# Performance work log

Measured on AMD Instinct MI355X. Metric: run time of the kernel, lower is better.

The kernel has to match this reference:

```python
import jax, jax.numpy as jnp
import numpy as np

EPS = 1e-5   # BatchNorm eps (torch default)
KNN_K = 9    # kernel_size * dilation
GROUPS = 4

def _bn(x, g, b, m, v):
    # channel-first BN in eval mode (running stats)
    shp = (1, -1) + (1,) * (x.ndim - 2)
    return (x - m.reshape(shp)) * (g.reshape(shp) * jax.lax.rsqrt(v.reshape(shp) + EPS)) + b.reshape(shp)

def setup_inputs() -> dict:
    key = jax.random.key(0)
    ks = jax.random.split(key, 16)
    B, C, H, W = 64, 192, 28, 28
    C2 = 2 * C
    d = {}
    d["x"] = jax.random.normal(ks[0], (B, C, H, W), jnp.float32)
    # fc1: Conv2d(C,C,1) + BN
    d["fc1_w"] = jax.random.normal(ks[1], (C, C), jnp.float32) * 0.05
    d["fc1_b"] = jnp.zeros((C,), jnp.float32)
    d["bn1_g"] = jnp.ones((C,), jnp.float32)
    d["bn1_b"] = jnp.zeros((C,), jnp.float32)
    d["bn1_m"] = jax.random.normal(ks[2], (C,), jnp.float32) * 0.1
    d["bn1_v"] = jax.random.uniform(ks[3], (C,), jnp.float32, 0.5, 1.5)
    # MRConv2d nn: grouped Conv2d(2C, 2C, 1, groups=4) + BN + GELU
    d["gc_w"] = jax.random.normal(ks[4], (GROUPS, C2 // GROUPS, C2 // GROUPS), jnp.float32) * 0.1  # (g, out/g, in/g)
    d["gc_b"] = jnp.zeros((C2,), jnp.float32)
    d["bn2_g"] = jnp.ones((C2,), jnp.float32)
    d["bn2_b"] = jnp.zeros((C2,), jnp.float32)
    d["bn2_m"] = jax.random.normal(ks[5], (C2,), jnp.float32) * 0.1
    d["bn2_v"] = jax.random.uniform(ks[6], (C2,), jnp.float32, 0.5, 1.5)
    # fc2: Conv2d(2C, C, 1) + BN
    d["fc2_w"] = jax.random.normal(ks[7], (C, C2), jnp.float32) * 0.05
    d["fc2_b"] = jnp.zeros((C,), jnp.float32)
    d["bn3_g"] = jnp.ones((C,), jnp.float32)
    d["bn3_b"] = jnp.zeros((C,), jnp.float32)
    d["bn3_m"] = jax.random.normal(ks[8], (C,), jnp.float32) * 0.1
    d["bn3_v"] = jax.random.uniform(ks[9], (C,), jnp.float32, 0.5, 1.5)
    return d

def reference(x, fc1_w, fc1_b, bn1_g, bn1_b, bn1_m, bn1_v,
              gc_w, gc_b, bn2_g, bn2_b, bn2_m, bn2_v,
              fc2_w, fc2_b, bn3_g, bn3_b, bn3_m, bn3_v):
    B, C, H, W = x.shape
    N = H * W
    shortcut = x
    # fc1 (1x1 conv + BN)
    h = jnp.einsum('bchw,oc->bohw', x, fc1_w) + fc1_b[None, :, None, None]
    h = _bn(h, bn1_g, bn1_b, bn1_m, bn1_v)
    xt = h.reshape(B, C, N)  # (B, C, N), r=1 so y == x.detach()
    # ---- dynamic KNN graph (no grad in original) ----
    xs = jax.lax.stop_gradient(xt)
    norm = jnp.maximum(jnp.linalg.norm(xs, axis=1, keepdims=True), 1e-12)
    xn = xs / norm                      # L2 normalize over channels
    p = jnp.swapaxes(xn, 1, 2)          # (B, N, C)
    sq = jnp.sum(p * p, axis=-1, keepdims=True)       # (B, N, 1)
    dist = sq - 2.0 * jnp.einsum('bnc,bmc->bnm', p, p) + jnp.swapaxes(sq, 1, 2)
    _, nn_idx = jax.lax.top_k(-dist, KNN_K)           # (B, N, K) smallest distances
    # ---- max-relative graph conv ----
    yd = jax.lax.stop_gradient(xt)      # neighbors come from detached y
    x_j = jax.vmap(lambda f, i: f[:, i])(yd, nn_idx)  # (B, C, N, K)
    mr = jnp.max(x_j - xt[..., None], axis=-1)        # (B, C, N)
    # interleave [x_c0, mr_c0, x_c1, mr_c1, ...] -> (B, 2C, N)
    st = jnp.stack([xt, mr], axis=2).reshape(B, 2 * C, N)
    # grouped 1x1 conv (groups=4)
    z = st.reshape(B, GROUPS, (2 * C) // GROUPS, N)
    g = jnp.einsum('bgin,goi->bgon', z, gc_w).reshape(B, 2 * C, N) + gc_b[None, :, None]
    g = _bn(g, bn2_g, bn2_b, bn2_m, bn2_v)
    g = jax.nn.gelu(g, approximate=False)
    g = g.reshape(B, 2 * C, H, W)
    # fc2 (1x1 conv + BN) + residual
    out = jnp.einsum('bchw,oc->bohw', g, fc2_w) + fc2_b[None, :, None, None]
    out = _bn(out, bn3_g, bn3_b, bn3_m, bn3_v)
    return out + shortcut
```

## Files before the change

### kernel.cpp

```cpp
#include <hip/hip_runtime.h>
#include <math.h>

static constexpr int Bn  = 64;
static constexpr int Cc  = 192;
static constexpr int Nn  = 784;
static constexpr int C2c = 384;
static constexpr int Kk  = 9;
#define GAP_DELTA 1e-4f

typedef __attribute__((ext_vector_type(8))) short bf16x8;
typedef __attribute__((ext_vector_type(4))) float f32x4;

__device__ inline unsigned short f2bf(float f) {
    unsigned int u = __float_as_uint(f);
    return (unsigned short)((u + 0x7FFFu + ((u >> 16) & 1u)) >> 16);
}


__global__ __launch_bounds__(256) void fc1_np(
    const float* __restrict__ x, const float* __restrict__ w,
    const float* __restrict__ bias,
    const float* __restrict__ gg, const float* __restrict__ bb_,
    const float* __restrict__ mm, const float* __restrict__ vv,
    float* __restrict__ xt)
{
    __shared__ float As[16][64];
    __shared__ float Bs[16][128];
    const int b   = blockIdx.z;
    const int n0  = blockIdx.x * 128;
    const int o0  = blockIdx.y * 64;
    const int tid = threadIdx.x;
    const int tx = tid & 15, ty = tid >> 4;
    const int lo = tid & 63, lk4 = tid >> 6;
    const int ln4 = tid & 15, lbk = tid >> 4;
    const float* xb = x + (size_t)b * Cc * Nn;

    float acc[4][8];
#pragma unroll
    for (int i = 0; i < 4; ++i)
#pragma unroll
        for (int j = 0; j < 8; ++j) acc[i][j] = 0.f;

    for (int kt = 0; kt < 12; ++kt) {
        const int k0 = kt * 16;
        float4 av = *reinterpret_cast<const float4*>(&w[(size_t)(o0 + lo) * 192 + k0 + lk4 * 4]);
        As[lk4*4+0][lo] = av.x;
        As[lk4*4+1][lo] = av.y;
        As[lk4*4+2][lo] = av.z;
        As[lk4*4+3][lo] = av.w;
        const int na = n0 + ln4 * 4;
        const int nb = n0 + 64 + ln4 * 4;
        float4 b0 = make_float4(0.f, 0.f, 0.f, 0.f);
        float4 b1 = make_float4(0.f, 0.f, 0.f, 0.f);
        if (na < Nn) b0 = *reinterpret_cast<const float4*>(&xb[(size_t)(k0 + lbk) * Nn + na]);
        if (nb < Nn) b1 = *reinterpret_cast<const float4*>(&xb[(size_t)(k0 + lbk) * Nn + nb]);
        *reinterpret_cast<float4*>(&Bs[lbk][ln4*4])      = b0;
        *reinterpret_cast<float4*>(&Bs[lbk][64 + ln4*4]) = b1;
        __syncthreads();
#pragma unroll
        for (int kk = 0; kk < 16; ++kk) {
            float ar[4], br[8];
#pragma unroll
            for (int i = 0; i < 4; ++i) ar[i] = As[kk][ty*4+i];
#pragma unroll
            for (int j = 0; j < 4; ++j) br[j]     = Bs[kk][tx*4+j];
#pragma unroll
            for (int j = 0; j < 4; ++j) br[4 + j] = Bs[kk][64 + tx*4+j];
#pragma unroll
            for (int i = 0; i < 4; ++i)
#pragma unroll
                for (int j = 0; j < 8; ++j)
                    acc[i][j] = __fadd_rn(acc[i][j], __fmul_rn(ar[i], br[j]));
        }
        __syncthreads();
    }
    const int na = n0 + tx * 4;
    const int nb = n0 + 64 + tx * 4;
#pragma unroll
    for (int i = 0; i < 4; ++i) {
        const int o = o0 + ty * 4 + i;
        const float e  = __fadd_rn(vv[o], 1e-5f);
        const float r1 = __fsqrt_rn(e);
        const float rr = __fdiv_rn(1.f, r1);
        const float s  = __fmul_rn(gg[o], rr);
        const size_t rowb = ((size_t)b * Cc + o) * Nn;
        if (na < Nn) {
#pragma unroll
            for (int j = 0; j < 4; ++j) {
                const float h = __fadd_rn(acc[i][j], bias[o]);
                const float t = __fsub_rn(h, mm[o]);
                const float u = __fmul_rn(t, s);
                xt[rowb + na + j] = __fadd_rn(u, bb_[o]);
            }
        }
        if (nb < Nn) {
#pragma unroll
            for (int j = 0; j < 4; ++j) {
                const float h = __fadd_rn(acc[i][4 + j], bias[o]);
                const float t = __fsub_rn(h, mm[o]);
                const float u = __fmul_rn(t, s);
                xt[rowb + nb + j] = __fadd_rn(u, bb_[o]);
            }
        }
    }
}

__global__ __launch_bounds__(256) void norm_np(
    const float* __restrict__ xt, float* __restrict__ xn, float* __restrict__ sq)
{
    const int idx = blockIdx.x * 256 + threadIdx.x;
    if (idx >= Bn * Nn) return;
    const int n = idx % Nn;
    const int b = idx / Nn;
    const float* p = xt + (size_t)b * Cc * Nn + n;

    float acc = 0.f;
    for (int c = 0; c < Cc; ++c) {
        const float v = p[(size_t)c * Nn];
        acc = __fadd_rn(acc, __fmul_rn(v, v));
    }
    float nrm = __fsqrt_rn(acc);
    nrm = fmaxf(nrm, 1e-12f);

    float* q = xn + (size_t)b * Cc * Nn + n;
    for (int c = 0; c < Cc; ++c)
        q[(size_t)c * Nn] = __fdiv_rn(p[(size_t)c * Nn], nrm);

    float sblk[2];
#pragma unroll
    for (int blk = 0; blk < 2; ++blk) {
        const int base = blk * 96;
        float r[8];
#pragma unroll
        for (int j = 0; j < 8; ++j) {
            const float xv = q[(size_t)(base + j) * Nn];
            r[j] = __fmul_rn(xv, xv);
        }
        for (int i = 8; i < 96; i += 8) {
#pragma unroll
            for (int j = 0; j < 8; ++j) {
                const float xv = q[(size_t)(base + i + j) * Nn];
                r[j] = __fadd_rn(r[j], __fmul_rn(xv, xv));
            }
        }
        sblk[blk] = __fadd_rn(__fadd_rn(__fadd_rn(r[0], r[1]), __fadd_rn(r[2], r[3])),
                              __fadd_rn(__fadd_rn(r[4], r[5]), __fadd_rn(r[6], r[7])));
    }
    sq[idx] = __fadd_rn(sblk[0], sblk[1]);
}

__global__ __launch_bounds__(256) void xpose_bf(
    const float* __restrict__ xn, unsigned short* __restrict__ xnh,
    unsigned short* __restrict__ xnl)
{
    __shared__ float T[64][65];
    const int b  = blockIdx.z;
    const int c0 = blockIdx.y * 64;
    const int n0 = blockIdx.x * 64;
    const int tid = threadIdx.x;
    const int nl = tid & 63, cq = tid >> 6;

#pragma unroll
    for (int i = 0; i < 16; ++i) {
        const int c = c0 + cq + i * 4;
        const int n = n0 + nl;
        T[cq + i*4][nl] = (n < Nn) ? xn[((size_t)b * Cc + c) * Nn + n] : 0.f;
    }
    __syncthreads();
    const int nw = tid >> 2, cpart = tid & 3;
    const int n = n0 + nw;
    if (n < Nn) {
        unsigned short hbuf[16], lbuf[16];
#pragma unroll
        for (int j = 0; j < 16; ++j) {
            const float v = T[cpart * 16 + j][nw];
            const unsigned short h = f2bf(v);
            const float hf = __uint_as_float(((unsigned int)h) << 16);
            hbuf[j] = h;
            lbuf[j] = f2bf(__fsub_rn(v, hf));
        }
        unsigned short* dh = xnh + ((size_t)b * Nn + n) * Cc + c0 + cpart * 16;
        unsigned short* dl = xnl + ((size_t)b * Nn + n) * Cc + c0 + cpart * 16;
        *reinterpret_cast<bf16x8*>(&dh[0]) = *reinterpret_cast<bf16x8*>(&hbuf[0]);
        *reinterpret_cast<bf16x8*>(&dh[8]) = *reinterpret_cast<bf16x8*>(&hbuf[8]);
        *reinterpret_cast<bf16x8*>(&dl[0]) = *reinterpret_cast<bf16x8*>(&lbuf[0]);
        *reinterpret_cast<bf16x8*>(&dl[8]) = *reinterpret_cast<bf16x8*>(&lbuf[8]);
    }
}

__global__ __launch_bounds__(256) void xpose_f32(
    const float* __restrict__ xn, float* __restrict__ xnT)
{
    __shared__ float T[64][65];
    const int b  = blockIdx.z;
    const int c0 = blockIdx.y * 64;
    const int n0 = blockIdx.x * 64;
    const int tid = threadIdx.x;
    const int nl = tid & 63, cq = tid >> 6;

#pragma unroll
    for (int i = 0; i < 16; ++i) {
        const int c = c0 + cq + i * 4;
        const int n = n0 + nl;
        T[cq + i*4][nl] = (n < Nn) ? xn[((size_t)b * Cc + c) * Nn + n] : 0.f;
    }
    __syncthreads();
    const int nw = tid >> 2, cpart = tid & 3;
    const int n = n0 + nw;
    if (n < Nn) {
        float* dst = xnT + ((size_t)b * Nn + n) * Cc + c0 + cpart * 16;
#pragma unroll
        for (int q = 0; q < 4; ++q) {
            float4 v = make_float4(T[cpart*16 + q*4 + 0][nw], T[cpart*16 + q*4 + 1][nw],
                                   T[cpart*16 + q*4 + 2][nw], T[cpart*16 + q*4 + 3][nw]);
            *reinterpret_cast<float4*>(&dst[q * 4]) = v;
        }
    }
}

__global__ __launch_bounds__(256) void dist_mfma(
    const unsigned short* __restrict__ xnh, const unsigned short* __restrict__ xnl,
    float* __restrict__ dist, int bchunk)
{
    __shared__ float Ds[64][65];
    __shared__ unsigned short Ah[64 * 40];
    __shared__ unsigned short Al[64 * 40];
    const int bt = blockIdx.x;
    int rt = 0, rem = bt;
    while (rem >= 13 - rt) { rem -= 13 - rt; ++rt; }
    const int mt = rt + rem;
    const int bc = blockIdx.y;
    const int b  = bchunk * 16 + bc;
    const int r0 = rt * 64, m0 = mt * 64;
    const int tid = threadIdx.x;
    const int wv = tid >> 6, l = tid & 63;
    const int lm = l & 15, lk = l >> 4;

    const int mcol = m0 + wv * 16 + lm;
    const int mcl  = (mcol < Nn) ? mcol : (Nn - 1);
    const unsigned short* mh = xnh + ((size_t)b * Nn + mcl) * Cc;
    const unsigned short* ml = xnl + ((size_t)b * Nn + mcl) * Cc;

    const int srow = tid >> 2, spart = tid & 3;
    const int arow = r0 + srow;
    const int arowc = (arow < Nn) ? arow : (Nn - 1);
    const unsigned short* ah_src = xnh + ((size_t)b * Nn + arowc) * Cc;
    const unsigned short* al_src = xnl + ((size_t)b * Nn + arowc) * Cc;

    f32x4 acc[4];
#pragma unroll
    for (int mf = 0; mf < 4; ++mf) acc[mf] = (f32x4){0.f, 0.f, 0.f, 0.f};

#pragma unroll
    for (int ks = 0; ks < 6; ++ks) {
        const int k0 = ks * 32;
        bf16x8 bh = *reinterpret_cast<const bf16x8*>(&mh[k0 + lk * 8]);
        bf16x8 bl = *reinterpret_cast<const bf16x8*>(&ml[k0 + lk * 8]);
        __syncthreads();
        *reinterpret_cast<bf16x8*>(&Ah[srow * 40 + spart * 8]) =
            *reinterpret_cast<const bf16x8*>(&ah_src[k0 + spart * 8]);
        *reinterpret_cast<bf16x8*>(&Al[srow * 40 + spart * 8]) =
            *reinterpret_cast<const bf16x8*>(&al_src[k0 + spart * 8]);
        __syncthreads();
#pragma unroll
        for (int mf = 0; mf < 4; ++mf) {
            bf16x8 ah = *reinterpret_cast<const bf16x8*>(&Ah[(mf * 16 + lm) * 40 + lk * 8]);
            bf16x8 al = *reinterpret_cast<const bf16x8*>(&Al[(mf * 16 + lm) * 40 + lk * 8]);
            acc[mf] = __builtin_amdgcn_mfma_f32_16x16x32_bf16(ah, bh, acc[mf], 0, 0, 0);
            acc[mf] = __builtin_amdgcn_mfma_f32_16x16x32_bf16(ah, bl, acc[mf], 0, 0, 0);
            acc[mf] = __builtin_amdgcn_mfma_f32_16x16x32_bf16(al, bh, acc[mf], 0, 0, 0);
        }
    }
    float* db = dist + (size_t)bc * Nn * Nn;
    __syncthreads();
#pragma unroll
    for (int mf = 0; mf < 4; ++mf) {
#pragma unroll
        for (int r = 0; r < 4; ++r) {
            const int rl = mf * 16 + lk * 4 + r;
            const float val = -acc[mf][r];
            Ds[rl][wv * 16 + lm] = val;
            const int rrow = r0 + rl;
            if (rrow < Nn && mcol < Nn)
                db[(size_t)rrow * Nn + mcol] = val;
        }
    }
    if (rt != mt) {
        __syncthreads();
        const int tx = tid & 15, ty = tid >> 4;
        const int rcol = r0 + tx * 4;
#pragma unroll
        for (int i = 0; i < 4; ++i) {
            const int mrow = m0 + ty * 4 + i;
            if (mrow < Nn) {
                float4 o = make_float4(Ds[tx*4+0][ty*4+i], Ds[tx*4+1][ty*4+i],
                                       Ds[tx*4+2][ty*4+i], Ds[tx*4+3][ty*4+i]);
                *reinterpret_cast<float4*>(&db[(size_t)mrow * Nn + rcol]) = o;
            }
        }
    }
}

__global__ __launch_bounds__(256) void select16(
    const float* __restrict__ dist, int* __restrict__ cand,
    float* __restrict__ cdist, int bchunk)
{
    const int wid = blockIdx.x * 4 + (threadIdx.x >> 6);
    const int L   = threadIdx.x & 63;
    const int r   = wid % Nn;
    const int bc  = wid / Nn;
    const int b   = bchunk * 16 + bc;
    const float* drow = dist + ((size_t)bc * Nn + r) * Nn;

    float v[13];
#pragma unroll
    for (int s = 0; s < 12; ++s) v[s] = drow[s * 64 + L];
    v[12] = (L < 16) ? drow[768 + L] : INFINITY;

    float mv = v[0]; int ms = 0;
#pragma unroll
    for (int s = 1; s < 13; ++s)
        if (v[s] < mv) { mv = v[s]; ms = s; }

    int out[16];
    float vals[16];
#pragma unroll
    for (int k = 0; k < 16; ++k) {
        float gv = mv; int gi = ms * 64 + L;
#pragma unroll
        for (int off = 1; off < 64; off <<= 1) {
            const float ov = __shfl_xor(gv, off, 64);
            const int   oi = __shfl_xor(gi, off, 64);
            if (ov < gv || (ov == gv && oi < gi)) { gv = ov; gi = oi; }
        }
        out[k] = gi; vals[k] = gv;
        const int ol = gi & 63, os = gi >> 6;
        if (L == ol) {
#pragma unroll
            for (int s = 0; s < 13; ++s) if (s == os) v[s] = INFINITY;
            mv = v[0]; ms = 0;
#pragma unroll
            for (int s = 1; s < 13; ++s)
                if (v[s] < mv) { mv = v[s]; ms = s; }
        }
    }
    if (L == 0) {
        int*   op = cand  + ((size_t)b * Nn + r) * 16;
        float* dp = cdist + ((size_t)b * Nn + r) * 16;
#pragma unroll
        for (int k = 0; k < 16; ++k) { op[k] = out[k]; dp[k] = vals[k]; }
    }
}

__global__ void zero_cnt(int* cnt) { if (threadIdx.x == 0 && blockIdx.x == 0) *cnt = 0; }

__global__ __launch_bounds__(256) void gap_route(
    const int* __restrict__ cand, const float* __restrict__ cdist,
    int* __restrict__ nnidx, int* __restrict__ amb, int* __restrict__ cnt)
{
    const int idx = blockIdx.x * 256 + threadIdx.x;
    if (idx >= Bn * Nn) return;
    const float* dp = cdist + (size_t)idx * 16;
    const float d8 = dp[8], d9 = dp[9];
    if (d9 - d8 > GAP_DELTA) {
        const int* cp = cand + (size_t)idx * 16;
        int* op = nnidx + (size_t)idx * Kk;
#pragma unroll
        for (int k = 0; k < Kk; ++k) op[k] = cp[k];
    } else {
        const int pos = atomicAdd(cnt, 1);
        amb[pos] = idx;
    }
}

__global__ __launch_bounds__(256) void refine_amb(
    const float* __restrict__ xnT, const float* __restrict__ sq,
    const int* __restrict__ cand, const int* __restrict__ amb,
    const int* __restrict__ cnt, int* __restrict__ nnidx)
{
    __shared__ float prods[16][200];
    __shared__ float Dd[16];
    __shared__ int   Dm[16];
    const int total = *cnt;
    const int k = threadIdx.x >> 4;
    const int j = threadIdx.x & 15;

    for (int row = blockIdx.x; row < total; row += gridDim.x) {
        const int rowid = amb[row];
        const int b = rowid / Nn, r = rowid % Nn;
        const float* sqb = sq + (size_t)b * Nn;
        const int m = cand[(size_t)rowid * 16 + k];
        const float* rT = xnT + ((size_t)b * Nn + r) * Cc;
        const float* mT = xnT + ((size_t)b * Nn + m) * Cc;

#pragma unroll
        for (int i = 0; i < 12; ++i) {
            const int c = j * 12 + i;
            prods[k][c] = __fmul_rn(rT[c], mT[c]);
        }
        __syncthreads();
        if (j == 0) {
            float dot = 0.f;
            for (int c = 0; c < Cc; ++c)
                dot = __fadd_rn(dot, prods[k][c]);
            const float t1 = __fmul_rn(2.f, dot);
            const float t2 = __fsub_rn(sqb[r], t1);
            Dd[k] = __fadd_rn(t2, sqb[m]);
            Dm[k] = m;
        }
        __syncthreads();
        if (threadIdx.x == 0) {
            float dl[16]; int il[16];
#pragma unroll
            for (int q = 0; q < 16; ++q) { dl[q] = Dd[q]; il[q] = Dm[q]; }
            int* op = nnidx + (size_t)rowid * Kk;
            for (int kk = 0; kk < Kk; ++kk) {
                int best = kk;
                for (int q = kk + 1; q < 16; ++q)
                    if (dl[q] < dl[best] || (dl[q] == dl[best] && il[q] < il[best])) best = q;
                float td = dl[kk]; dl[kk] = dl[best]; dl[best] = td;
                int ti = il[kk]; il[kk] = il[best]; il[best] = ti;
                op[kk] = il[kk];
            }
        }
        __syncthreads();
    }
}


__global__ __launch_bounds__(256) void mr_pack(
    const float* __restrict__ xt, const int* __restrict__ nnidx,
    unsigned int* __restrict__ stT)
{
    __shared__ float rows[16][784];
    const int b   = blockIdx.y;
    const int c0  = blockIdx.x * 16;
    const int tid = threadIdx.x;
    const float* xb = xt + ((size_t)b * Cc + c0) * Nn;

#pragma unroll
    for (int c = 0; c < 16; ++c)
        for (int n = tid; n < Nn; n += 256)
            rows[c][n] = xb[(size_t)c * Nn + n];
    __syncthreads();

    for (int n = tid; n < Nn; n += 256) {
        const int* ip = nnidx + ((size_t)b * Nn + n) * Kk;
        int idx[Kk];
#pragma unroll
        for (int k = 0; k < Kk; ++k) idx[k] = ip[k];
        unsigned int pk[16];
#pragma unroll
        for (int c = 0; c < 16; ++c) {
            const float ctr = rows[c][n];
            float mx = -INFINITY;
#pragma unroll
            for (int k = 0; k < Kk; ++k)
                mx = fmaxf(mx, __fsub_rn(rows[c][idx[k]], ctr));
            pk[c] = (unsigned int)f2bf(ctr) | ((unsigned int)f2bf(mx) << 16);
        }
        unsigned int* dst = stT + ((size_t)b * Nn + n) * (C2c / 2) + c0;
#pragma unroll
        for (int q = 0; q < 4; ++q) {
            uint4 v = make_uint4(pk[q*4+0], pk[q*4+1], pk[q*4+2], pk[q*4+3]);
            *reinterpret_cast<uint4*>(&dst[q * 4]) = v;
        }
    }
}

__global__ __launch_bounds__(256) void wcvt(
    const float* __restrict__ w, unsigned short* __restrict__ wbf, int nElem)
{
    const int i = blockIdx.x * 256 + threadIdx.x;
    if (i < nElem) wbf[i] = f2bf(w[i]);
}

__global__ __launch_bounds__(256) void gconv_mfma(
    const unsigned short* __restrict__ stT, const unsigned short* __restrict__ wbf2,
    const float* __restrict__ gb,
    const float* __restrict__ gg, const float* __restrict__ bb_,
    const float* __restrict__ mm, const float* __restrict__ vv,
    unsigned short* __restrict__ gT)
{
    const int b   = blockIdx.z;
    const int grp = blockIdx.y;
    const int n0  = blockIdx.x * 64;
    const int tid = threadIdx.x;
    const int wv  = tid >> 6;
    const int l   = tid & 63;
    const int lm  = l & 15, lk = l >> 4;

    const int ncol = n0 + wv * 16 + lm;
    const int ncl  = (ncol < Nn) ? ncol : (Nn - 1);
    const unsigned short* gRow = stT + ((size_t)b * Nn + ncl) * C2c + grp * 96;

    f32x4 acc[6];
#pragma unroll
    for (int mf = 0; mf < 6; ++mf) acc[mf] = (f32x4){0.f, 0.f, 0.f, 0.f};

#pragma unroll
    for (int k0 = 0; k0 < 96; k0 += 32) {
        bf16x8 bfr = *reinterpret_cast<const bf16x8*>(&gRow[k0 + lk * 8]);
#pragma unroll
        for (int mf = 0; mf < 6; ++mf) {
            bf16x8 afr = *reinterpret_cast<const bf16x8*>(
                &wbf2[((size_t)grp * 96 + mf * 16 + lm) * 96 + k0 + lk * 8]);
            acc[mf] = __builtin_amdgcn_mfma_f32_16x16x32_bf16(afr, bfr, acc[mf], 0, 0, 0);
        }
    }
    if (ncol < Nn) {
#pragma unroll
        for (int mf = 0; mf < 6; ++mf) {
            unsigned long long pk = 0ull;
#pragma unroll
            for (int r = 0; r < 4; ++r) {
                const int oc = grp * 96 + mf * 16 + lk * 4 + r;
                const float s  = gg[oc] * rsqrtf(vv[oc] + 1e-5f);
                const float sh = (gb[oc] - mm[oc]) * s + bb_[oc];
                float v = fmaf(acc[mf][r], s, sh);
                float ge = 0.5f * v * (1.f + erff(v * 0.70710678118654752f));
                pk |= ((unsigned long long)f2bf(ge)) << (16 * r);
            }
            *reinterpret_cast<unsigned long long*>(
                &gT[((size_t)b * Nn + ncol) * C2c + grp * 96 + mf * 16 + lk * 4]) = pk;
        }
    }
}

__global__ __launch_bounds__(256) void fc2_mfma(
    const unsigned short* __restrict__ gT, const unsigned short* __restrict__ wbf,
    const float* __restrict__ bias,
    const float* __restrict__ gg, const float* __restrict__ bb_,
    const float* __restrict__ mm, const float* __restrict__ vv,
    const float* __restrict__ xres,
    float* __restrict__ out)
{
    __shared__ float sS[192], sH[192];
    __shared__ unsigned short sW[192 * 40];
    const int b   = blockIdx.y;
    const int n0  = blockIdx.x * 64;
    const int tid = threadIdx.x;
    const int wv  = tid >> 6;
    const int l   = tid & 63;
    const int lm  = l & 15, lk = l >> 4;

    if (tid < 192) {
        const float s = gg[tid] * rsqrtf(vv[tid] + 1e-5f);
        sS[tid] = s;
        sH[tid] = (bias[tid] - mm[tid]) * s + bb_[tid];
    }

    const int ncol = n0 + wv * 16 + lm;
    const int ncl  = (ncol < Nn) ? ncol : (Nn - 1);
    const unsigned short* gRow = gT + ((size_t)b * Nn + ncl) * C2c;

    f32x4 acc[12];
#pragma unroll
    for (int mf = 0; mf < 12; ++mf) acc[mf] = (f32x4){0.f, 0.f, 0.f, 0.f};

    const int srow = tid >> 2, spart = tid & 3;
    for (int ks = 0; ks < 12; ++ks) {
        const int k0 = ks * 32;
        bf16x8 bfr = *reinterpret_cast<const bf16x8*>(&gRow[k0 + lk * 8]);
        __syncthreads();
#pragma unroll
        for (int p = 0; p < 3; ++p) {
            const int row = srow + p * 64;
            *reinterpret_cast<bf16x8*>(&sW[row * 40 + spart * 8]) =
                *reinterpret_cast<const bf16x8*>(&wbf[(size_t)row * C2c + k0 + spart * 8]);
        }
        __syncthreads();
#pragma unroll
        for (int mf = 0; mf < 12; ++mf) {
            bf16x8 afr = *reinterpret_cast<const bf16x8*>(&sW[(mf * 16 + lm) * 40 + lk * 8]);
            acc[mf] = __builtin_amdgcn_mfma_f32_16x16x32_bf16(afr, bfr, acc[mf], 0, 0, 0);
        }
    }
    if (ncol < Nn) {
#pragma unroll
        for (int mf = 0; mf < 12; ++mf) {
#pragma unroll
            for (int r = 0; r < 4; ++r) {
                const int o = mf * 16 + lk * 4 + r;
                const size_t oi = ((size_t)b * Cc + o) * Nn + ncol;
                out[oi] = fmaf(acc[mf][r], sS[o], sH[o]) + xres[oi];
            }
        }
    }
}

extern "C" void kernel_launch(void* const* d_in, const int* in_sizes, int n_in,
                              void* d_out, int out_size, void* d_ws, size_t ws_size,
                              hipStream_t stream)
{
    const float* x     = (const float*)d_in[0];
    const float* fc1_w = (const float*)d_in[1];
    const float* fc1_b = (const float*)d_in[2];
    const float* bn1_g = (const float*)d_in[3];
    const float* bn1_b = (const float*)d_in[4];
    const float* bn1_m = (const float*)d_in[5];
    const float* bn1_v = (const float*)d_in[6];
    const float* gc_w  = (const float*)d_in[7];
    const float* gc_b  = (const float*)d_in[8];
    const float* bn2_g = (const float*)d_in[9];
    const float* bn2_b = (const float*)d_in[10];
    const float* bn2_m = (const float*)d_in[11];
    const float* bn2_v = (const float*)d_in[12];
    const float* fc2_w = (const float*)d_in[13];
    const float* fc2_b = (const float*)d_in[14];
    const float* bn3_g = (const float*)d_in[15];
    const float* bn3_b = (const float*)d_in[16];
    const float* bn3_m = (const float*)d_in[17];
    const float* bn3_v = (const float*)d_in[18];

    float* out = (float*)d_out;

    char* wsb = (char*)d_ws;
    const size_t regionBytes = (size_t)Bn * C2c * Nn * 4;
    const size_t distBytes   = (size_t)16 * Nn * Nn * 4;
    float* dist = (float*)wsb;
    unsigned short* xnh = (unsigned short*)(wsb + distBytes);
    float* xnT  = (float*)wsb;
    unsigned int*   stT32 = (unsigned int*)wsb;
    unsigned short* stT   = (unsigned short*)wsb;
    char*  g2   = wsb + regionBytes;
    float* xnb  = (float*)g2;
    float* sqb  = (float*)(g2 + (size_t)Bn * Cc * Nn * 4);
    int*   c16  = (int*)(g2 + (size_t)Bn * Cc * Nn * 4 + 200704);
    float* cd16 = (float*)(g2 + (size_t)Bn * Cc * Nn * 4 + 200704 + 3211264);
    unsigned short* gT   = (unsigned short*)g2;
    unsigned short* wbf  = (unsigned short*)(g2 + 45158912);
    unsigned short* wbf2 = (unsigned short*)(g2 + 45158912 + 147456);
    unsigned short* xnl  = (unsigned short*)(g2 + 45158912 + 147456 + 73728);
    char*  g3   = wsb + 2 * regionBytes;
    int*   nni  = (int*)g3;
    int*   amb  = (int*)(g3 + 1806336);
    int*   cnt  = (int*)(g3 + 1806336 + 200704);

    const int nBN = Bn * Nn;

    dim3 blk(256);
    wcvt<<<dim3((Cc * C2c + 255) / 256), blk, 0, stream>>>(fc2_w, wbf, Cc * C2c);
    wcvt<<<dim3((4 * 96 * 96 + 255) / 256), blk, 0, stream>>>(gc_w, wbf2, 4 * 96 * 96);
    fc1_np<<<dim3(7, 3, Bn), blk, 0, stream>>>(
        x, fc1_w, fc1_b, bn1_g, bn1_b, bn1_m, bn1_v, out);
    norm_np<<<dim3((nBN + 255) / 256), blk, 0, stream>>>(out, xnb, sqb);
    xpose_bf<<<dim3(13, 3, Bn), blk, 0, stream>>>(xnb, xnh, xnl);
    for (int ch = 0; ch < 4; ++ch) {
        dist_mfma<<<dim3(91, 16), blk, 0, stream>>>(xnh, xnl, dist, ch);
        select16<<<dim3(16 * Nn / 4), blk, 0, stream>>>(dist, c16, cd16, ch);
    }
    xpose_f32<<<dim3(13, 3, Bn), blk, 0, stream>>>(xnb, xnT);
    zero_cnt<<<dim3(1), dim3(64), 0, stream>>>(cnt);
    gap_route<<<dim3((nBN + 255) / 256), blk, 0, stream>>>(c16, cd16, nni, amb, cnt);
    refine_amb<<<dim3(784), blk, 0, stream>>>(xnT, sqb, c16, amb, cnt, nni);
    mr_pack<<<dim3(12, Bn), blk, 0, stream>>>(out, nni, stT32);
    gconv_mfma<<<dim3(13, 4, Bn), blk, 0, stream>>>(
        stT, wbf2, gc_b, bn2_g, bn2_b, bn2_m, bn2_v, gT);
    fc2_mfma<<<dim3(13, Bn), blk, 0, stream>>>(
        gT, wbf, fc2_b, bn3_g, bn3_b, bn3_m, bn3_v, x, out);
}
```

Measured before the change: 550.8 us.

## Fuse L2 normalization with bf16 split and f32 transpose into one kernel

Replaces norm_np, xpose_bf and xpose_f32 with a single norm_fuse kernel. It loads a 192x64 tile of fc1 output into shared memory, computes norms, normalizes in place, computes squared norms, and writes the bf16 hi/lo and f32 transposed layouts directly. This removes the intermediate normalized array and two extra global read passes. The fused kernel uses about 50KB of shared memory per block, which may reduce occupancy, and it runs only 832 blocks with serial per-column norm loops on 64 threads.

After: 522.3 us. 5.2% less time.

```diff
diff --git a/kernel.cpp b/kernel.cpp
--- a/kernel.cpp
+++ b/kernel.cpp
@@ -105,115 +105,104 @@
     }
 }
 
-__global__ __launch_bounds__(256) void norm_np(
-    const float* __restrict__ xt, float* __restrict__ xn, float* __restrict__ sq)
-{
-    const int idx = blockIdx.x * 256 + threadIdx.x;
-    if (idx >= Bn * Nn) return;
-    const int n = idx % Nn;
-    const int b = idx / Nn;
-    const float* p = xt + (size_t)b * Cc * Nn + n;
-
-    float acc = 0.f;
-    for (int c = 0; c < Cc; ++c) {
-        const float v = p[(size_t)c * Nn];
-        acc = __fadd_rn(acc, __fmul_rn(v, v));
-    }
-    float nrm = __fsqrt_rn(acc);
-    nrm = fmaxf(nrm, 1e-12f);
-
-    float* q = xn + (size_t)b * Cc * Nn + n;
-    for (int c = 0; c < Cc; ++c)
-        q[(size_t)c * Nn] = __fdiv_rn(p[(size_t)c * Nn], nrm);
-
-    float sblk[2];
-#pragma unroll
-    for (int blk = 0; blk < 2; ++blk) {
-        const int base = blk * 96;
-        float r[8];
-#pragma unroll
-        for (int j = 0; j < 8; ++j) {
-            const float xv = q[(size_t)(base + j) * Nn];
-            r[j] = __fmul_rn(xv, xv);
-        }
-        for (int i = 8; i < 96; i += 8) {
-#pragma unroll
-            for (int j = 0; j < 8; ++j) {
-                const float xv = q[(size_t)(base + i + j) * Nn];
-                r[j] = __fadd_rn(r[j], __fmul_rn(xv, xv));
-            }
-        }
-        sblk[blk] = __fadd_rn(__fadd_rn(__fadd_rn(r[0], r[1]), __fadd_rn(r[2], r[3])),
-                              __fadd_rn(__fadd_rn(r[4], r[5]), __fadd_rn(r[6], r[7])));
-    }
-    sq[idx] = __fadd_rn(sblk[0], sblk[1]);
-}
-
-__global__ __launch_bounds__(256) void xpose_bf(
-    const float* __restrict__ xn, unsigned short* __restrict__ xnh,
-    unsigned short* __restrict__ xnl)
-{
-    __shared__ float T[64][65];
-    const int b  = blockIdx.z;
-    const int c0 = blockIdx.y * 64;
-    const int n0 = blockIdx.x * 64;
+__global__ __launch_bounds__(256) void norm_fuse(
+    const float* __restrict__ xt,
+    unsigned short* __restrict__ xnh, unsigned short* __restrict__ xnl,
+    float* __restrict__ xnT, float* __restrict__ sq)
+{
+    __shared__ float T[192][65];
+    __shared__ float nrmv[64];
+    const int b   = blockIdx.y;
+    const int n0  = blockIdx.x * 64;
     const int tid = threadIdx.x;
-    const int nl = tid & 63, cq = tid >> 6;
-
-#pragma unroll
-    for (int i = 0; i < 16; ++i) {
-        const int c = c0 + cq + i * 4;
-        const int n = n0 + nl;
-        T[cq + i*4][nl] = (n < Nn) ? xn[((size_t)b * Cc + c) * Nn + n] : 0.f;
+    const float* xb = xt + (size_t)b * Cc * Nn;
+
+    for (int t = tid; t < 192 * 16; t += 256) {
+        const int c = t >> 4, part = t & 15;
+        const int n = n0 + part * 4;
+        float4 v = make_float4(0.f, 0.f, 0.f, 0.f);
+        if (n < Nn) v = *reinterpret_cast<const float4*>(&xb[(size_t)c * Nn + n]);
+        T[c][part*4+0] = v.x; T[c][part*4+1] = v.y;
+        T[c][part*4+2] = v.z; T[c][part*4+3] = v.w;
     }
     __syncthreads();
+
+    if (tid < 64) {
+        const int n = n0 + tid;
+        float nrm = 1.f;
+        if (n < Nn) {
+            float acc = 0.f;
+            for (int c = 0; c < Cc; ++c) {
+                const float v = T[c][tid];
+                acc = __fadd_rn(acc, __fmul_rn(v, v));
+            }
+            nrm = __fsqrt_rn(acc);
+            nrm = fmaxf(nrm, 1e-12f);
+        }
+        nrmv[tid] = nrm;
+    }
+    __syncthreads();
+
+    for (int t = tid; t < 192 * 64; t += 256) {
+        const int c = t >> 6, nl = t & 63;
+        T[c][nl] = __fdiv_rn(T[c][nl], nrmv[nl]);
+    }
+    __syncthreads();
+
+    if (tid < 64) {
+        const int n = n0 + tid;
+        if (n < Nn) {
+            float sblk[2];
+#pragma unroll
+            for (int blk = 0; blk < 2; ++blk) {
+                const int base = blk * 96;
+                float r[8];
+#pragma unroll
+                for (int j = 0; j < 8; ++j) {
+                    const float xv = T[base + j][tid];
+                    r[j] = __fmul_rn(xv, xv);
+                }
+                for (int i = 8; i < 96; i += 8) {
+#pragma unroll
+                    for (int j = 0; j < 8; ++j) {
+                        const float xv = T[base + i + j][tid];
+                        r[j] = __fadd_rn(r[j], __fmul_rn(xv, xv));
+                    }
+                }
+                sblk[blk] = __fadd_rn(
+                    __fadd_rn(__fadd_rn(r[0], r[1]), __fadd_rn(r[2], r[3])),
+                    __fadd_rn(__fadd_rn(r[4], r[5]), __fadd_rn(r[6], r[7])));
+            }
+            sq[b * Nn + n] = __fadd_rn(sblk[0], sblk[1]);
+        }
+    }
+
     const int nw = tid >> 2, cpart = tid & 3;
     const int n = n0 + nw;
     if (n < Nn) {
-        unsigned short hbuf[16], lbuf[16];
-#pragma unroll
-        for (int j = 0; j < 16; ++j) {
-            const float v = T[cpart * 16 + j][nw];
+        const int cbase = cpart * 48;
+        float* dT = xnT + ((size_t)b * Nn + n) * Cc + cbase;
+#pragma unroll
+        for (int q = 0; q < 12; ++q) {
+            float4 v = make_float4(T[cbase + q*4 + 0][nw], T[cbase + q*4 + 1][nw],
+                                   T[cbase + q*4 + 2][nw], T[cbase + q*4 + 3][nw]);
+            *reinterpret_cast<float4*>(&dT[q * 4]) = v;
+        }
+        unsigned short hbuf[48], lbuf[48];
+#pragma unroll
+        for (int j = 0; j < 48; ++j) {
+            const float v = T[cbase + j][nw];
             const unsigned short h = f2bf(v);
             const float hf = __uint_as_float(((unsigned int)h) << 16);
             hbuf[j] = h;
             lbuf[j] = f2bf(__fsub_rn(v, hf));
         }
-        unsigned short* dh = xnh + ((size_t)b * Nn + n) * Cc + c0 + cpart * 16;
-        unsigned short* dl = xnl + ((size_t)b * Nn + n) * Cc + c0 + cpart * 16;
-        *reinterpret_cast<bf16x8*>(&dh[0]) = *reinterpret_cast<bf16x8*>(&hbuf[0]);
-        *reinterpret_cast<bf16x8*>(&dh[8]) = *reinterpret_cast<bf16x8*>(&hbuf[8]);
-        *reinterpret_cast<bf16x8*>(&dl[0]) = *reinterpret_cast<bf16x8*>(&lbuf[0]);
-        *reinterpret_cast<bf16x8*>(&dl[8]) = *reinterpret_cast<bf16x8*>(&lbuf[8]);
-    }
-}
-
-__global__ __launch_bounds__(256) void xpose_f32(
-    const float* __restrict__ xn, float* __restrict__ xnT)
-{
-    __shared__ float T[64][65];
-    const int b  = blockIdx.z;
-    const int c0 = blockIdx.y * 64;
-    const int n0 = blockIdx.x * 64;
-    const int tid = threadIdx.x;
-    const int nl = tid & 63, cq = tid >> 6;
-
-#pragma unroll
-    for (int i = 0; i < 16; ++i) {
-        const int c = c0 + cq + i * 4;
-        const int n = n0 + nl;
-        T[cq + i*4][nl] = (n < Nn) ? xn[((size_t)b * Cc + c) * Nn + n] : 0.f;
-    }
-    __syncthreads();
-    const int nw = tid >> 2, cpart = tid & 3;
-    const int n = n0 + nw;
-    if (n < Nn) {
-        float* dst = xnT + ((size_t)b * Nn + n) * Cc + c0 + cpart * 16;
-#pragma unroll
-        for (int q = 0; q < 4; ++q) {
-            float4 v = make_float4(T[cpart*16 + q*4 + 0][nw], T[cpart*16 + q*4 + 1][nw],
-                                   T[cpart*16 + q*4 + 2][nw], T[cpart*16 + q*4 + 3][nw]);
-            *reinterpret_cast<float4*>(&dst[q * 4]) = v;
+        unsigned short* dh = xnh + ((size_t)b * Nn + n) * Cc + cbase;
+        unsigned short* dl = xnl + ((size_t)b * Nn + n) * Cc + cbase;
+#pragma unroll
+        for (int q = 0; q < 6; ++q) {
+            *reinterpret_cast<bf16x8*>(&dh[q * 8]) = *reinterpret_cast<bf16x8*>(&hbuf[q * 8]);
+            *reinterpret_cast<bf16x8*>(&dl[q * 8]) = *reinterpret_cast<bf16x8*>(&lbuf[q * 8]);
         }
     }
 }
@@ -620,11 +609,10 @@
     const size_t distBytes   = (size_t)16 * Nn * Nn * 4;
     float* dist = (float*)wsb;
     unsigned short* xnh = (unsigned short*)(wsb + distBytes);
-    float* xnT  = (float*)wsb;
     unsigned int*   stT32 = (unsigned int*)wsb;
     unsigned short* stT   = (unsigned short*)wsb;
     char*  g2   = wsb + regionBytes;
-    float* xnb  = (float*)g2;
+    float* xnT  = (float*)g2;
     float* sqb  = (float*)(g2 + (size_t)Bn * Cc * Nn * 4);
     int*   c16  = (int*)(g2 + (size_t)Bn * Cc * Nn * 4 + 200704);
     float* cd16 = (float*)(g2 + (size_t)Bn * Cc * Nn * 4 + 200704 + 3211264);
@@ -644,13 +632,11 @@
     wcvt<<<dim3((4 * 96 * 96 + 255) / 256), blk, 0, stream>>>(gc_w, wbf2, 4 * 96 * 96);
     fc1_np<<<dim3(7, 3, Bn), blk, 0, stream>>>(
         x, fc1_w, fc1_b, bn1_g, bn1_b, bn1_m, bn1_v, out);
-    norm_np<<<dim3((nBN + 255) / 256), blk, 0, stream>>>(out, xnb, sqb);
-    xpose_bf<<<dim3(13, 3, Bn), blk, 0, stream>>>(xnb, xnh, xnl);
+    norm_fuse<<<dim3(13, Bn), blk, 0, stream>>>(out, xnh, xnl, xnT, sqb);
     for (int ch = 0; ch < 4; ++ch) {
         dist_mfma<<<dim3(91, 16), blk, 0, stream>>>(xnh, xnl, dist, ch);
         select16<<<dim3(16 * Nn / 4), blk, 0, stream>>>(dist, c16, cd16, ch);
     }
-    xpose_f32<<<dim3(13, 3, Bn), blk, 0, stream>>>(xnb, xnT);
     zero_cnt<<<dim3(1), dim3(64), 0, stream>>>(cnt);
     gap_route<<<dim3((nBN + 255) / 256), blk, 0, stream>>>(c16, cd16, nni, amb, cnt);
     refine_amb<<<dim3(784), blk, 0, stream>>>(xnT, sqb, c16, amb, cnt, nni);
```
